# Kernel tuning notes

Hardware: AMD Instinct MI355X
Metric: run time of the kernel (lower is better)

## Reference

```python
import jax, jax.numpy as jnp
import numpy as np

B, G, C = 32, 50, 80
IMG = 640
STRIDES = (8, 16, 32)
CENTER_RADIUS = 2.5


def _make_grids():
    xs, ys, ss = [], [], []
    for s in STRIDES:
        n = IMG // s
        yv, xv = np.meshgrid(np.arange(n, dtype=np.float32), np.arange(n, dtype=np.float32), indexing='ij')
        xs.append(xv.reshape(-1)); ys.append(yv.reshape(-1))
        ss.append(np.full(n * n, s, dtype=np.float32))
    return np.concatenate(xs), np.concatenate(ys), np.concatenate(ss)


def setup_inputs():
    xg, yg, sg = _make_grids()
    A = xg.shape[0]  # 8400
    ks = jax.random.split(jax.random.key(0), 5)
    # decoded box predictions near grid centers (cxcywh, pixel units)
    ctr = jnp.stack([jnp.asarray((xg + 0.5) * sg), jnp.asarray((yg + 0.5) * sg)], -1)[None] \
        + jax.random.normal(ks[0], (B, A, 2)) * 8.0
    wh = jnp.exp(jax.random.normal(ks[1], (B, A, 2)) * 0.5) * jnp.asarray(sg)[None, :, None] * 4.0
    pred_output = jnp.concatenate([ctr, wh, jax.random.normal(ks[2], (B, A, 1 + C))], -1)  # [B,A,85]
    obj_preds = jax.random.normal(ks[3], (B, A, 1))
    cls_preds = jax.random.normal(ks[4], (B, A, C))
    # labels [B,G,5] = (class, cx, cy, w, h); first num_gt rows valid, rest zero
    rng = np.random.RandomState(0)
    lab = np.zeros((B, G, 5), np.float32)
    for b in range(B):
        ng = rng.randint(5, G)
        lab[b, :ng, 0] = rng.randint(0, C, ng)
        lab[b, :ng, 1:3] = rng.uniform(40.0, IMG - 40.0, (ng, 2))
        lab[b, :ng, 3:5] = rng.uniform(20.0, 160.0, (ng, 2))
    return {"pred_output": pred_output, "obj_preds": obj_preds, "cls_preds": cls_preds,
            "labels": jnp.asarray(lab), "x_shifts": jnp.asarray(xg),
            "y_shifts": jnp.asarray(yg), "strides": jnp.asarray(sg)}


def _pairwise_iou_cxcywh(a, b):
    # a [G,4], b [A,4] -> [G,A]
    tl = jnp.maximum(a[:, None, :2] - a[:, None, 2:] * 0.5, b[None, :, :2] - b[None, :, 2:] * 0.5)
    br = jnp.minimum(a[:, None, :2] + a[:, None, 2:] * 0.5, b[None, :, :2] + b[None, :, 2:] * 0.5)
    area_a = a[:, 2] * a[:, 3]
    area_b = b[:, 2] * b[:, 3]
    en = jnp.all(tl < br, -1).astype(a.dtype)
    area_i = jnp.prod(br - tl, -1) * en
    return area_i / (area_a[:, None] + area_b[None, :] - area_i + 1e-16)


def _assign_one(gt, gt_valid, boxes, cls_logit, obj_logit, xg, yg, sg):
    # SimOTA assignment for a single image, fully vectorized over [G,A].
    # gt [G,5], gt_valid [G], boxes [A,4], cls_logit [A,C], obj_logit [A,1]
    num_gt = gt.shape[0]
    gt_cls = gt[:, 0].astype(jnp.int32)
    gb = gt[:, 1:5]
    xc = (xg + 0.5) * sg
    yc = (yg + 0.5) * sg
    d_box = jnp.stack([
        xc[None, :] - (gb[:, 0:1] - gb[:, 2:3] * 0.5),
        (gb[:, 0:1] + gb[:, 2:3] * 0.5) - xc[None, :],
        yc[None, :] - (gb[:, 1:2] - gb[:, 3:4] * 0.5),
        (gb[:, 1:2] + gb[:, 3:4] * 0.5) - yc[None, :]], -1)
    in_boxes = (jnp.min(d_box, -1) > 0) & gt_valid[:, None]
    d_ctr = jnp.stack([
        xc[None, :] - (gb[:, 0:1] - CENTER_RADIUS * sg[None, :]),
        (gb[:, 0:1] + CENTER_RADIUS * sg[None, :]) - xc[None, :],
        yc[None, :] - (gb[:, 1:2] - CENTER_RADIUS * sg[None, :]),
        (gb[:, 1:2] + CENTER_RADIUS * sg[None, :]) - yc[None, :]], -1)
    in_ctr = (jnp.min(d_ctr, -1) > 0) & gt_valid[:, None]
    fg0 = jnp.any(in_boxes | in_ctr, 0)           # [A] candidate anchors (fg_mask)
    and_ctr = in_boxes & in_ctr                    # [G,A]
    ious = _pairwise_iou_cxcywh(gb, boxes) * fg0[None, :].astype(boxes.dtype) * gt_valid[:, None].astype(boxes.dtype)
    # pairwise BCE(sqrt(sig(cls)*sig(obj)), one_hot) summed over classes, without [G,A,C]
    logq = 0.5 * (jax.nn.log_sigmoid(cls_logit) + jax.nn.log_sigmoid(obj_logit))  # [A,C]
    q = jnp.clip(jnp.exp(logq), 1e-7, 1.0 - 1e-7)
    s_neg = jnp.sum(jnp.log1p(-q), -1)             # [A] sum_c log(1-q_c)
    q_gt = q[:, gt_cls].T                          # [G,A]
    cls_cost = -jnp.log(q_gt) + jnp.log1p(-q_gt) - s_neg[None, :]
    invalid = (~fg0)[None, :] | (~gt_valid)[:, None]
    cost = cls_cost - 3.0 * jnp.log(ious + 1e-8) + 1e5 * (~and_ctr) + 1e9 * invalid
    # dynamic-k: sum of top-10 ious per gt, truncated, min 1
    dyn_k = jnp.maximum(jnp.sum(jax.lax.top_k(ious, 10)[0], -1).astype(jnp.int32), 1)  # [G]
    ranks = jnp.argsort(jnp.argsort(cost, 1), 1)   # rank of each anchor in ascending cost
    matching = (ranks < dyn_k[:, None]) & gt_valid[:, None]
    # resolve anchors claimed by >1 gt: keep min-cost gt
    best_gt = jnp.argmin(cost, 0)                  # [A]
    onehot_best = jnp.arange(num_gt)[:, None] == best_gt[None, :]
    matching = jnp.where(jnp.sum(matching, 0)[None, :] > 1, onehot_best, matching)
    fg = jnp.any(matching, 0)                      # [A] final fg mask
    matched = jnp.argmax(matching, 0)              # [A] matched gt index
    pred_iou = jnp.sum(matching * ious, 0)         # [A]
    cls_t = jax.nn.one_hot(gt_cls[matched], cls_logit.shape[-1], dtype=boxes.dtype) \
        * (pred_iou * fg.astype(boxes.dtype))[:, None]
    return cls_t, fg, matched


def _forward(pred_output, obj_preds, cls_preds, labels, x_shifts, y_shifts, strides):
    bbox = pred_output[:, :, :4]
    gt_valid = labels.sum(-1) > 0
    cls_t, fg, matched = jax.vmap(_assign_one, in_axes=(0, 0, 0, 0, 0, None, None, None))(
        labels, gt_valid, bbox, cls_preds, obj_preds, x_shifts, y_shifts, strides)
    cls_t = jax.lax.stop_gradient(cls_t)  # get_assignments is @torch.no_grad()
    reg_t = jnp.take_along_axis(labels[:, :, 1:5], matched[:, :, None], axis=1)  # [B,A,4]
    fg_f = fg.astype(pred_output.dtype)
    num_fg = jnp.maximum(jnp.sum(fg_f), 1.0)
    # IoU loss (cxcywh), loss = 1 - iou^2, only on fg anchors
    tl = jnp.maximum(bbox[..., :2] - bbox[..., 2:] * 0.5, reg_t[..., :2] - reg_t[..., 2:] * 0.5)
    br = jnp.minimum(bbox[..., :2] + bbox[..., 2:] * 0.5, reg_t[..., :2] + reg_t[..., 2:] * 0.5)
    en = jnp.all(tl < br, -1).astype(bbox.dtype)
    area_i = jnp.prod(br - tl, -1) * en
    area_u = bbox[..., 2] * bbox[..., 3] + reg_t[..., 2] * reg_t[..., 3] - area_i
    iou = area_i / (area_u + 1e-16)
    loss_iou = jnp.sum((1.0 - iou ** 2) * fg_f) / num_fg
    bce = lambda x, y: jax.nn.softplus(x) - x * y  # BCEWithLogits, reduction='none'
    loss_obj = jnp.sum(bce(obj_preds[..., 0], fg_f)) / num_fg
    loss_cls = jnp.sum(bce(cls_preds, cls_t) * fg_f[..., None]) / num_fg
    return 5.0 * loss_iou + loss_obj + loss_cls


def reference(pred_output, obj_preds, cls_preds, labels, x_shifts, y_shifts, strides):
    return _forward(pred_output, obj_preds, cls_preds, labels, x_shifts, y_shifts, strides)
```

## Files before the change

kernel.cpp:

```cpp
#include <hip/hip_runtime.h>
#include <cstdint>
#include <cstddef>

#define BB 32
#define GG 50
#define CC 80
#define AA 8400
#define PCH (5 + CC)
#define NLB ((BB * AA + 255) / 256)
#define FGBIT 63
#define SENTC 3.3e38f
#define SENTI 0x7fffffff

__device__ __forceinline__ float logsig_fast(float x) {
    float e = __expf(-fabsf(x));
    return fminf(x, 0.f) - __logf(1.f + e);
}
__device__ __forceinline__ float softplusf(float x) {
    return fmaxf(x, 0.f) + log1pf(expf(-fabsf(x)));
}

__device__ __forceinline__ float pair_iou(float px, float py, float pw, float ph,
                                          float gx, float gy, float gw, float gh) {
    float tlx = fmaxf(gx - gw * 0.5f, px - pw * 0.5f);
    float tly = fmaxf(gy - gh * 0.5f, py - ph * 0.5f);
    float brx = fminf(gx + gw * 0.5f, px + pw * 0.5f);
    float bry = fminf(gy + gh * 0.5f, py + ph * 0.5f);
    float en = (tlx < brx && tly < bry) ? 1.f : 0.f;
    float ai = (brx - tlx) * (bry - tly) * en;
    return ai / (gw * gh + pw * ph - ai + 1e-16f);
}
__device__ __forceinline__ float cost_val(float x , float lo ,
                                          float sn , float v ,
                                          bool ac, bool f0, bool valid) {
    float lq = 0.5f * (logsig_fast(x) + lo);
    float q = fminf(fmaxf(__expf(lq), 1e-7f), 1.f - 1e-7f);
    float cst = -__logf(q) + __logf(1.f - q) - sn;
    cst -= 3.0f * __logf(v + 1e-8f);
    cst += 100000.0f * (ac ? 0.f : 1.f);
    cst += 1000000000.0f * ((!f0 || !valid) ? 1.f : 0.f);
    return cst;
}

__global__ void k_geom(const float* __restrict__ labels, const float* __restrict__ xs,
                       const float* __restrict__ ys, const float* __restrict__ ss,
                       const float* __restrict__ pred,
                       unsigned long long* __restrict__ amask,
                       int* __restrict__ clist, unsigned long long* __restrict__ camask,
                       float4* __restrict__ cpbox, int* __restrict__ ccnt) {
    int b = blockIdx.y;
    int a = blockIdx.x * blockDim.x + threadIdx.x;
    __shared__ float lab[GG * 5];
    __shared__ int lv[GG];
    for (int t = threadIdx.x; t < GG * 5; t += blockDim.x) lab[t] = labels[b * GG * 5 + t];
    __syncthreads();
    if (threadIdx.x < GG) {
        const float* r = lab + threadIdx.x * 5;
        lv[threadIdx.x] = ((r[0] + r[1] + r[2] + r[3] + r[4]) > 0.f) ? 1 : 0;
    }
    __syncthreads();
    if (a >= AA) return;
    float s = ss[a];
    float xc = (xs[a] + 0.5f) * s;
    float yc = (ys[a] + 0.5f) * s;
    unsigned long long m = 0;
    int any = 0;
    for (int g = 0; g < GG; g++) {
        if (!lv[g]) continue;
        const float* r = lab + g * 5;
        float gx = r[1], gy = r[2], gw = r[3], gh = r[4];
        float d1 = xc - (gx - gw * 0.5f);
        float d2 = (gx + gw * 0.5f) - xc;
        float d3 = yc - (gy - gh * 0.5f);
        float d4 = (gy + gh * 0.5f) - yc;
        bool ib = fminf(fminf(d1, d2), fminf(d3, d4)) > 0.f;
        float cr = 2.5f * s;
        float e1 = xc - (gx - cr);
        float e2 = (gx + cr) - xc;
        float e3 = yc - (gy - cr);
        float e4 = (gy + cr) - yc;
        bool ic = fminf(fminf(e1, e2), fminf(e3, e4)) > 0.f;
        if (ib || ic) any = 1;
        if (ib && ic) m |= 1ull << g;
    }
    if (any) m |= 1ull << FGBIT;
    amask[b * AA + a] = m;
    int lane = threadIdx.x & 63;
    unsigned long long act = __ballot(m != 0);
    if (act) {
        int leader = __ffsll(act) - 1;
        int base = 0;
        if (lane == leader) base = atomicAdd(&ccnt[b], __popcll(act));
        base = __shfl(base, leader);
        if (m != 0) {
            int off = __popcll(act & ((1ull << lane) - 1ull));
            int pos = b * AA + base + off;
            clist[pos] = a;
            camask[pos] = m;
            const float* p = pred + (size_t)(b * AA + a) * PCH;
            cpbox[pos] = make_float4(p[0], p[1], p[2], p[3]);
        }
    }
}

__global__ __launch_bounds__(256)
void k_pre_fg(const float* __restrict__ obj, const float* __restrict__ cls,
              const int* __restrict__ clist, const int* __restrict__ ccnt,
              float2* __restrict__ clsn, float2* __restrict__ lsn,
              float* __restrict__ sps) {
    int b = blockIdx.y;
    int cnt = ccnt[b];
    int t = blockIdx.x * blockDim.x + threadIdx.x;
    int p = t >> 2;
    int sub = t & 3;
    if (p >= cnt) return;
    int pos = b * AA + p;
    int a = clist[pos];
    int ia = b * AA + a;
    float lo = logsig_fast(obj[ia]);
    float K = __expf(0.5f * lo);
    const float4* c4 = (const float4*)(cls + (size_t)ia * CC);
    float smax = 0.f, psp = 1.f, p1 = 1.f, p2 = 1.f;
#pragma unroll
    for (int j = 0; j < 5; j++) {
        float4 v = c4[sub + 4 * j];
        float xs4[4] = {v.x, v.y, v.z, v.w};
        float pg = 1.f;
#pragma unroll
        for (int u = 0; u < 4; u++) {
            float x = xs4[u];
            float th = __expf(-0.5f * fabsf(x));
            float t2 = th * th;
            smax += fmaxf(x, 0.f);
            psp *= (1.f + t2);
            float qq = K * (x < 0.f ? th : 1.f) * rsqrtf(1.f + t2);
            qq = fminf(fmaxf(qq, 1e-7f), 1.f - 1e-7f);
            pg *= (1.f - qq);
        }
        if (j < 2) p1 *= pg; else p2 *= pg;
    }
    float sp = smax + __logf(psp);
    float sn = __logf(p1) + __logf(p2);
    sp += __shfl_xor(sp, 1); sn += __shfl_xor(sn, 1);
    sp += __shfl_xor(sp, 2); sn += __shfl_xor(sn, 2);
    if (sub == 0) {
        clsn[pos] = make_float2(lo, sn);
        lsn[ia] = make_float2(lo, sn);
        sps[ia] = sp;
    }
}

__global__ __launch_bounds__(256, 4)
void k_assign(const float* __restrict__ pred, const float2* __restrict__ lsn,
              const float* __restrict__ cls,
              const unsigned long long* __restrict__ amask,
              const float* __restrict__ labels,
              const int* __restrict__ clist, const unsigned long long* __restrict__ camask,
              const float4* __restrict__ cpbox, const float2* __restrict__ clsn,
              const int* __restrict__ ccnt,
              unsigned long long* __restrict__ mmask) {
    int w = blockIdx.x;
    int b = w / GG, g = w % GG;
    const float* r = labels + (size_t)w * 5;
    float gcls = r[0], gx = r[1], gy = r[2], gw = r[3], gh = r[4];
    if (!((gcls + gx + gy + gw + gh) > 0.f)) return;
    int gtc = (int)gcls;
    int tid = threadIdx.x;
    int lane = tid & 63;
    int wv = tid >> 6;
    int cnt = ccnt[b];

    float ivl[10];
    float cvl[10];
    int   cil[10];
#pragma unroll
    for (int t = 0; t < 10; t++) { ivl[t] = 0.f; cvl[t] = SENTC; cil[t] = SENTI; }
    int nlc = 0;

    for (int i0 = wv * 64 + lane; i0 < cnt; i0 += 256) {
        int pos = b * AA + i0;
        unsigned long long am = camask[pos];
        float4 pb = cpbox[pos];
        bool ac = (am >> g) & 1ull;
        nlc += ac ? 1 : 0;
        float v = pair_iou(pb.x, pb.y, pb.z, pb.w, gx, gy, gw, gh);
        if (v > ivl[9]) {
            float mv = v;
#pragma unroll
            for (int t = 0; t < 10; t++)
                if (mv > ivl[t]) { float tmp = ivl[t]; ivl[t] = mv; mv = tmp; }
        }
        if (ac) {
            int a = clist[pos];
            float2 ls = clsn[pos];
            float c = cost_val(cls[((size_t)b * AA + a) * CC + gtc], ls.x, ls.y, v,
                               true, true, true);
            int id = a;
            if (c < cvl[9] || (c == cvl[9] && id < cil[9])) {
#pragma unroll
                for (int t = 0; t < 10; t++) {
                    bool sw = (c < cvl[t]) || (c == cvl[t] && id < cil[t]);
                    if (sw) {
                        float tf = cvl[t]; cvl[t] = c; c = tf;
                        int ti = cil[t]; cil[t] = id; id = ti;
                    }
                }
            }
        }
    }

    __shared__ float IV[4][10];
    __shared__ float CV[4][10];
    __shared__ int CI[4][10];
    __shared__ int NAC[4];
    __shared__ int s_k, s_n0;
    __shared__ int sel[10];

    {
        int s = nlc;
#pragma unroll
        for (int off = 1; off < 64; off <<= 1) s += __shfl_xor(s, off);
        if (lane == 0) NAC[wv] = s;
    }

    for (int rr = 0; rr < 10; rr++) {
        float bv = ivl[0];
        int bl = lane;
#pragma unroll
        for (int off = 1; off < 64; off <<= 1) {
            float ov = __shfl_xor(bv, off);
            int ol = __shfl_xor(bl, off);
            if (ov > bv || (ov == bv && ol < bl)) { bv = ov; bl = ol; }
        }
        if (lane == 0) IV[wv][rr] = bv;
        if (lane == bl) {
#pragma unroll
            for (int t = 0; t < 9; t++) ivl[t] = ivl[t + 1];
            ivl[9] = 0.f;
        }
    }

    for (int rr = 0; rr < 10; rr++) {
        float bc = cvl[0];
        int bi = cil[0];
        int bl = lane;
#pragma unroll
        for (int off = 1; off < 64; off <<= 1) {
            float oc = __shfl_xor(bc, off);
            int oi = __shfl_xor(bi, off);
            int ol = __shfl_xor(bl, off);
            bool tk = (oc < bc) || (oc == bc && (oi < bi || (oi == bi && ol < bl)));
            if (tk) { bc = oc; bi = oi; bl = ol; }
        }
        if (lane == 0) { CV[wv][rr] = bc; CI[wv][rr] = bi; }
        if (lane == bl) {
#pragma unroll
            for (int t = 0; t < 9; t++) { cvl[t] = cvl[t + 1]; cil[t] = cil[t + 1]; }
            cvl[9] = SENTC; cil[9] = SENTI;
        }
    }
    __syncthreads();

    if (tid == 0) {
        int h[4] = {0, 0, 0, 0};
        float ssum = 0.f;
        for (int j = 0; j < 10; j++) {
            float bv = -1.f; int bc = 0;
#pragma unroll
            for (int c2 = 0; c2 < 4; c2++)
                if (h[c2] < 10 && IV[c2][h[c2]] > bv) { bv = IV[c2][h[c2]]; bc = c2; }
            ssum += bv;
            h[bc]++;
        }
        int k = (int)ssum;
        if (k < 1) k = 1;
        s_k = k;
        s_n0 = NAC[0] + NAC[1] + NAC[2] + NAC[3];
    }
    __syncthreads();
    int k = s_k;

    if (s_n0 < k) {
#pragma unroll
        for (int t = 0; t < 10; t++) { cvl[t] = SENTC; cil[t] = SENTI; }
        const int chunk = AA / 4;
        int abase = wv * chunk, aend = abase + chunk;
        for (int a0 = abase; a0 < aend; a0 += 64) {
            int a = a0 + lane;
            bool inr = a < aend;
            int ia = b * AA + (inr ? a : (aend - 1));
            unsigned long long am = amask[ia];
            bool f0 = inr && ((am >> FGBIT) & 1ull);
            bool ac = inr && ((am >> g) & 1ull);
            float v = 0.f;
            if (f0) {
                const float* p = pred + (size_t)ia * PCH;
                v = pair_iou(p[0], p[1], p[2], p[3], gx, gy, gw, gh);
            }
            float c = SENTC; int id = SENTI;
            if (inr) {
                float x = cls[(size_t)ia * CC + gtc];
                float2 ls = lsn[ia];
                c = cost_val(x, ls.x, ls.y, v, ac, f0, true);
                id = a;
            }
            if (c < cvl[9] || (c == cvl[9] && id < cil[9])) {
#pragma unroll
                for (int t = 0; t < 10; t++) {
                    bool sw = (c < cvl[t]) || (c == cvl[t] && id < cil[t]);
                    if (sw) {
                        float tf = cvl[t]; cvl[t] = c; c = tf;
                        int ti = cil[t]; cil[t] = id; id = ti;
                    }
                }
            }
        }
        for (int rr = 0; rr < 10; rr++) {
            float bc = cvl[0];
            int bi = cil[0];
            int bl = lane;
#pragma unroll
            for (int off = 1; off < 64; off <<= 1) {
                float oc = __shfl_xor(bc, off);
                int oi = __shfl_xor(bi, off);
                int ol = __shfl_xor(bl, off);
                bool tk = (oc < bc) || (oc == bc && (oi < bi || (oi == bi && ol < bl)));
                if (tk) { bc = oc; bi = oi; bl = ol; }
            }
            if (lane == 0) { CV[wv][rr] = bc; CI[wv][rr] = bi; }
            if (lane == bl) {
#pragma unroll
                for (int t = 0; t < 9; t++) { cvl[t] = cvl[t + 1]; cil[t] = cil[t + 1]; }
                cvl[9] = SENTC; cil[9] = SENTI;
            }
        }
        __syncthreads();
    }

    if (tid == 0) {
        int h[4] = {0, 0, 0, 0};
        for (int j = 0; j < k; j++) {
            float bv = SENTC; int bix = SENTI; int bc = 0;
#pragma unroll
            for (int c2 = 0; c2 < 4; c2++) {
                if (h[c2] < 10) {
                    float av = CV[c2][h[c2]]; int ax = CI[c2][h[c2]];
                    if (av < bv || (av == bv && ax < bix)) { bv = av; bix = ax; bc = c2; }
                }
            }
            sel[j] = bix;
            h[bc]++;
        }
    }
    __syncthreads();
    if (tid < k) {
        atomicOr(&mmask[(size_t)b * AA + sel[tid]], 1ull << g);
    }
}

__global__ void k_loss(const float* __restrict__ pred, const float* __restrict__ obj,
                       const float* __restrict__ cls, const float* __restrict__ labels,
                       const float2* __restrict__ lsn,
                       const unsigned long long* __restrict__ amask,
                       const unsigned long long* __restrict__ mmask,
                       const float* __restrict__ sps, float* __restrict__ partial) {
    int i = blockIdx.x * blockDim.x + threadIdx.x;
    int i_first = blockIdx.x * blockDim.x;
    int i_last = min(i_first + (int)blockDim.x - 1, BB * AA - 1);
    int b0 = i_first / AA, b1 = i_last / AA;
    __shared__ float lab[2][GG * 5];
    for (int t = threadIdx.x; t < GG * 5; t += blockDim.x) {
        lab[0][t] = labels[(size_t)b0 * GG * 5 + t];
        lab[1][t] = labels[(size_t)b1 * GG * 5 + t];
    }
    __syncthreads();

    float li = 0.f, lo = 0.f, lc = 0.f, nf = 0.f;
    if (i < BB * AA) {
        int b = i / AA, a = i % AA;
        const float* lb = lab[(b == b0) ? 0 : 1];
        unsigned long long m = mmask[i];
        int cnt = __popcll(m);
        bool fg = (m != 0);
        int mg = 0;
        float4 pb = make_float4(0.f, 0.f, 0.f, 0.f);
        if (fg) {
            const float* p = pred + (size_t)i * PCH;
            pb = make_float4(p[0], p[1], p[2], p[3]);
        }
        unsigned long long am = amask[i];
        bool f0 = (am >> FGBIT) & 1ull;
        if (cnt > 1) {
            float2 ls = lsn[i];
            float bv = 3.4e38f;
            for (int g = 0; g < GG; g++) {
                const float* r = lb + g * 5;
                float gcls = r[0], gx = r[1], gy = r[2], gw = r[3], gh = r[4];
                bool valid = (gcls + gx + gy + gw + gh) > 0.f;
                int gtc = (int)gcls;
                float raw = pair_iou(pb.x, pb.y, pb.z, pb.w, gx, gy, gw, gh);
                float v = raw * (f0 ? 1.f : 0.f) * (valid ? 1.f : 0.f);
                float x = cls[(size_t)i * CC + gtc];
                bool ac = (am >> g) & 1ull;
                float cst = cost_val(x, ls.x, ls.y, v, ac, f0, valid);
                if (cst < bv) { bv = cst; mg = g; }
            }
        } else if (cnt == 1) {
            mg = __ffsll((unsigned long long)m) - 1;
        }
        float o = obj[i];
        lo = softplusf(o) - (fg ? o : 0.f);
        if (fg) {
            const float* r = lb + mg * 5;
            float gcls = r[0], gx = r[1], gy = r[2], gw = r[3], gh = r[4];
            bool valid = (gcls + gx + gy + gw + gh) > 0.f;
            int gtc = (int)gcls;
            float piou = pair_iou(pb.x, pb.y, pb.z, pb.w, gx, gy, gw, gh)
                         * (f0 ? 1.f : 0.f) * (valid ? 1.f : 0.f);
            float tlx = fmaxf(pb.x - pb.z * 0.5f, gx - gw * 0.5f);
            float tly = fmaxf(pb.y - pb.w * 0.5f, gy - gh * 0.5f);
            float brx = fminf(pb.x + pb.z * 0.5f, gx + gw * 0.5f);
            float bry = fminf(pb.y + pb.w * 0.5f, gy + gh * 0.5f);
            float en = (tlx < brx && tly < bry) ? 1.f : 0.f;
            float ai = (brx - tlx) * (bry - tly) * en;
            float u = pb.z * pb.w + gw * gh - ai;
            float v2 = ai / (u + 1e-16f);
            li = 1.f - v2 * v2;
            lc = sps[i] - cls[(size_t)i * CC + gtc] * piou;
            nf = 1.f;
        }
    }
    for (int off = 32; off; off >>= 1) {
        li += __shfl_down(li, off);
        lo += __shfl_down(lo, off);
        lc += __shfl_down(lc, off);
        nf += __shfl_down(nf, off);
    }
    __shared__ float red[4][4];
    int wid = threadIdx.x >> 6;
    if ((threadIdx.x & 63) == 0) {
        red[wid][0] = li; red[wid][1] = lo; red[wid][2] = lc; red[wid][3] = nf;
    }
    __syncthreads();
    if (threadIdx.x == 0) {
        float s0 = 0.f, s1 = 0.f, s2 = 0.f, s3 = 0.f;
#pragma unroll
        for (int t = 0; t < 4; t++) {
            s0 += red[t][0]; s1 += red[t][1]; s2 += red[t][2]; s3 += red[t][3];
        }
        ((float4*)partial)[blockIdx.x] = make_float4(s0, s1, s2, s3);
    }
}

__global__ void k_final(const float* __restrict__ partial, float* __restrict__ out) {
    int tid = threadIdx.x;
    float s0 = 0.f, s1 = 0.f, s2 = 0.f, s3 = 0.f;
    const float4* pb = (const float4*)partial;
    for (int i = tid; i < NLB; i += 256) {
        float4 v = pb[i];
        s0 += v.x; s1 += v.y; s2 += v.z; s3 += v.w;
    }
    for (int off = 32; off; off >>= 1) {
        s0 += __shfl_down(s0, off);
        s1 += __shfl_down(s1, off);
        s2 += __shfl_down(s2, off);
        s3 += __shfl_down(s3, off);
    }
    __shared__ float red[4][4];
    int wid = tid >> 6;
    if ((tid & 63) == 0) {
        red[wid][0] = s0; red[wid][1] = s1; red[wid][2] = s2; red[wid][3] = s3;
    }
    __syncthreads();
    if (tid == 0) {
        float li = 0.f, lo = 0.f, lc = 0.f, nf = 0.f;
#pragma unroll
        for (int t = 0; t < 4; t++) {
            li += red[t][0]; lo += red[t][1]; lc += red[t][2]; nf += red[t][3];
        }
        nf = fmaxf(nf, 1.f);
        out[0] = (5.f * li + lo + lc) / nf;
    }
}

extern "C" void kernel_launch(void* const* d_in, const int* in_sizes, int n_in,
                              void* d_out, int out_size, void* d_ws, size_t ws_size,
                              hipStream_t stream) {
    const float* pred = (const float*)d_in[0];
    const float* obj  = (const float*)d_in[1];
    const float* cls  = (const float*)d_in[2];
    const float* lab  = (const float*)d_in[3];
    const float* xs   = (const float*)d_in[4];
    const float* ys   = (const float*)d_in[5];
    const float* ss   = (const float*)d_in[6];
    float* out = (float*)d_out;

    const size_t BA = (size_t)BB * AA;

    float4* cpbox = (float4*)d_ws;
    float2* lsn   = (float2*)(cpbox + BA);
    float2* clsn  = lsn + BA;
    unsigned long long* amask  = (unsigned long long*)(clsn + BA);
    unsigned long long* camask = amask + BA;
    unsigned long long* mmask  = camask + BA;
    float* sps = (float*)(mmask + BA);
    float* partial = sps + BA;
    int* clist = (int*)(partial + (size_t)NLB * 4);
    int* ccnt  = clist + BA;

    hipMemsetAsync(mmask, 0, BA * sizeof(unsigned long long), stream);
    hipMemsetAsync(ccnt, 0, BB * sizeof(int), stream);

    dim3 blk(256);
    k_geom<<<dim3((AA + 255) / 256, BB), blk, 0, stream>>>(lab, xs, ys, ss, pred,
                                                           amask, clist, camask, cpbox,
                                                           ccnt);
    k_pre_fg<<<dim3((AA * 4 + 255) / 256, BB), blk, 0, stream>>>(obj, cls, clist, ccnt,
                                                                 clsn, lsn, sps);
    k_assign<<<dim3(BB * GG), blk, 0, stream>>>(pred, lsn, cls, amask, lab,
                                                clist, camask, cpbox, clsn, ccnt, mmask);
    k_loss<<<dim3(NLB), blk, 0, stream>>>(pred, obj, cls, lab, lsn, amask,
                                          mmask, sps, partial);
    k_final<<<1, blk, 0, stream>>>(partial, out);
}
```

Measured before the change: 143.2 us.

## Split per-GT assignment into two-half scan plus merge kernel

The per-GT dynamic-k assignment kernel is split into two kernels. The first scans the candidate list in two halves with a 2D grid (doubling block count) and writes per-half top-10 IoU and cost lists to workspace. The second, a single-wave block per GT, merges the two halves, computes k, and runs the rare fallback full scan with one wave. The aim is more parallelism in the candidate scan, at the cost of an extra launch, workspace round-trip, and a slower single-wave fallback path.

```diff
diff --git a/kernel.cpp b/kernel.cpp
--- a/kernel.cpp
+++ b/kernel.cpp
@@ -151,15 +151,15 @@
 }
 
 __global__ __launch_bounds__(256, 4)
-void k_assign(const float* __restrict__ pred, const float2* __restrict__ lsn,
-              const float* __restrict__ cls,
-              const unsigned long long* __restrict__ amask,
-              const float* __restrict__ labels,
-              const int* __restrict__ clist, const unsigned long long* __restrict__ camask,
-              const float4* __restrict__ cpbox, const float2* __restrict__ clsn,
-              const int* __restrict__ ccnt,
-              unsigned long long* __restrict__ mmask) {
+void k_assign1(const float* __restrict__ cls,
+               const unsigned long long* __restrict__ camask,
+               const float4* __restrict__ cpbox, const float2* __restrict__ clsn,
+               const int* __restrict__ clist, const int* __restrict__ ccnt,
+               const float* __restrict__ labels,
+               float* __restrict__ giou, float* __restrict__ gcost,
+               int* __restrict__ gidx, int* __restrict__ gnac) {
     int w = blockIdx.x;
+    int half = blockIdx.y;
     int b = w / GG, g = w % GG;
     const float* r = labels + (size_t)w * 5;
     float gcls = r[0], gx = r[1], gy = r[2], gw = r[3], gh = r[4];
@@ -169,6 +169,9 @@
     int lane = tid & 63;
     int wv = tid >> 6;
     int cnt = ccnt[b];
+    int hmid = (cnt + 1) >> 1;
+    int hstart = half ? hmid : 0;
+    int hend = half ? cnt : hmid;
 
     float ivl[10];
     float cvl[10];
@@ -177,7 +180,7 @@
     for (int t = 0; t < 10; t++) { ivl[t] = 0.f; cvl[t] = SENTC; cil[t] = SENTI; }
     int nlc = 0;
 
-    for (int i0 = wv * 64 + lane; i0 < cnt; i0 += 256) {
+    for (int i0 = hstart + wv * 64 + lane; i0 < hend; i0 += 256) {
         int pos = b * AA + i0;
         unsigned long long am = camask[pos];
         float4 pb = cpbox[pos];
@@ -213,8 +216,6 @@
     __shared__ float CV[4][10];
     __shared__ int CI[4][10];
     __shared__ int NAC[4];
-    __shared__ int s_k, s_n0;
-    __shared__ int sel[10];
 
     {
         int s = nlc;
@@ -239,7 +240,6 @@
             ivl[9] = 0.f;
         }
     }
-
     for (int rr = 0; rr < 10; rr++) {
         float bc = cvl[0];
         int bi = cil[0];
@@ -262,48 +262,102 @@
     __syncthreads();
 
     if (tid == 0) {
+        size_t obase = ((size_t)w * 2 + half) * 10;
         int h[4] = {0, 0, 0, 0};
+        for (int j = 0; j < 10; j++) {
+            float bv = -1.f; int bc = 0;
+#pragma unroll
+            for (int c2 = 0; c2 < 4; c2++)
+                if (h[c2] < 10 && IV[c2][h[c2]] > bv) { bv = IV[c2][h[c2]]; bc = c2; }
+            giou[obase + j] = bv;
+            h[bc]++;
+        }
+        h[0] = h[1] = h[2] = h[3] = 0;
+        for (int j = 0; j < 10; j++) {
+            float bv = SENTC; int bix = SENTI; int bc = 0;
+#pragma unroll
+            for (int c2 = 0; c2 < 4; c2++) {
+                if (h[c2] < 10) {
+                    float av = CV[c2][h[c2]]; int ax = CI[c2][h[c2]];
+                    if (av < bv || (av == bv && ax < bix)) { bv = av; bix = ax; bc = c2; }
+                }
+            }
+            gcost[obase + j] = bv;
+            gidx[obase + j] = bix;
+            h[bc]++;
+        }
+        gnac[w * 2 + half] = NAC[0] + NAC[1] + NAC[2] + NAC[3];
+    }
+}
+
+__global__ __launch_bounds__(64)
+void k_assign2(const float* __restrict__ labels,
+               const float* __restrict__ giou, const float* __restrict__ gcost,
+               const int* __restrict__ gidx, const int* __restrict__ gnac,
+               const float* __restrict__ pred, const float2* __restrict__ lsn,
+               const float* __restrict__ cls,
+               const unsigned long long* __restrict__ amask,
+               unsigned long long* __restrict__ mmask) {
+    int w = blockIdx.x;
+    int b = w / GG, g = w % GG;
+    const float* r = labels + (size_t)w * 5;
+    float gcls = r[0], gx = r[1], gy = r[2], gw = r[3], gh = r[4];
+    if (!((gcls + gx + gy + gw + gh) > 0.f)) return;
+    int gtc = (int)gcls;
+    int lane = threadIdx.x;
+
+    __shared__ int s_k, s_n0;
+    __shared__ int sel[10];
+
+    if (lane == 0) {
+        size_t o0 = (size_t)w * 2 * 10, o1 = o0 + 10;
+        int h0 = 0, h1 = 0;
         float ssum = 0.f;
         for (int j = 0; j < 10; j++) {
-            float bv = -1.f; int bc = 0;
-#pragma unroll
-            for (int c2 = 0; c2 < 4; c2++)
-                if (h[c2] < 10 && IV[c2][h[c2]] > bv) { bv = IV[c2][h[c2]]; bc = c2; }
-            ssum += bv;
-            h[bc]++;
+            float a0 = (h0 < 10) ? giou[o0 + h0] : -1.f;
+            float a1 = (h1 < 10) ? giou[o1 + h1] : -1.f;
+            if (a0 >= a1) { ssum += a0; h0++; }
+            else          { ssum += a1; h1++; }
         }
         int k = (int)ssum;
         if (k < 1) k = 1;
         s_k = k;
-        s_n0 = NAC[0] + NAC[1] + NAC[2] + NAC[3];
+        s_n0 = gnac[w * 2] + gnac[w * 2 + 1];
+        if (s_n0 >= k) {
+            h0 = h1 = 0;
+            for (int j = 0; j < k; j++) {
+                float a0 = (h0 < 10) ? gcost[o0 + h0] : SENTC;
+                int x0 = (h0 < 10) ? gidx[o0 + h0] : SENTI;
+                float a1 = (h1 < 10) ? gcost[o1 + h1] : SENTC;
+                int x1 = (h1 < 10) ? gidx[o1 + h1] : SENTI;
+                bool t0 = (a0 < a1) || (a0 == a1 && x0 < x1);
+                if (t0) { sel[j] = x0; h0++; }
+                else    { sel[j] = x1; h1++; }
+            }
+        }
     }
     __syncthreads();
     int k = s_k;
 
     if (s_n0 < k) {
+        float cvl[10];
+        int cil[10];
 #pragma unroll
         for (int t = 0; t < 10; t++) { cvl[t] = SENTC; cil[t] = SENTI; }
-        const int chunk = AA / 4;
-        int abase = wv * chunk, aend = abase + chunk;
-        for (int a0 = abase; a0 < aend; a0 += 64) {
-            int a = a0 + lane;
-            bool inr = a < aend;
-            int ia = b * AA + (inr ? a : (aend - 1));
+        for (int a = lane; a < AA; a += 64) {
+            int ia = b * AA + a;
             unsigned long long am = amask[ia];
-            bool f0 = inr && ((am >> FGBIT) & 1ull);
-            bool ac = inr && ((am >> g) & 1ull);
+            bool f0 = (am >> FGBIT) & 1ull;
+            bool ac = (am >> g) & 1ull;
             float v = 0.f;
             if (f0) {
                 const float* p = pred + (size_t)ia * PCH;
                 v = pair_iou(p[0], p[1], p[2], p[3], gx, gy, gw, gh);
             }
-            float c = SENTC; int id = SENTI;
-            if (inr) {
-                float x = cls[(size_t)ia * CC + gtc];
-                float2 ls = lsn[ia];
-                c = cost_val(x, ls.x, ls.y, v, ac, f0, true);
-                id = a;
-            }
+            float x = cls[(size_t)ia * CC + gtc];
+            float2 ls = lsn[ia];
+            float c = cost_val(x, ls.x, ls.y, v, ac, f0, true);
+            int id = a;
             if (c < cvl[9] || (c == cvl[9] && id < cil[9])) {
 #pragma unroll
                 for (int t = 0; t < 10; t++) {
@@ -315,7 +369,7 @@
                 }
             }
         }
-        for (int rr = 0; rr < 10; rr++) {
+        for (int rr = 0; rr < k; rr++) {
             float bc = cvl[0];
             int bi = cil[0];
             int bl = lane;
@@ -327,7 +381,7 @@
                 bool tk = (oc < bc) || (oc == bc && (oi < bi || (oi == bi && ol < bl)));
                 if (tk) { bc = oc; bi = oi; bl = ol; }
             }
-            if (lane == 0) { CV[wv][rr] = bc; CI[wv][rr] = bi; }
+            if (lane == 0) sel[rr] = bi;
             if (lane == bl) {
 #pragma unroll
                 for (int t = 0; t < 9; t++) { cvl[t] = cvl[t + 1]; cil[t] = cil[t + 1]; }
@@ -337,24 +391,8 @@
         __syncthreads();
     }
 
-    if (tid == 0) {
-        int h[4] = {0, 0, 0, 0};
-        for (int j = 0; j < k; j++) {
-            float bv = SENTC; int bix = SENTI; int bc = 0;
-#pragma unroll
-            for (int c2 = 0; c2 < 4; c2++) {
-                if (h[c2] < 10) {
-                    float av = CV[c2][h[c2]]; int ax = CI[c2][h[c2]];
-                    if (av < bv || (av == bv && ax < bix)) { bv = av; bix = ax; bc = c2; }
-                }
-            }
-            sel[j] = bix;
-            h[bc]++;
-        }
-    }
-    __syncthreads();
-    if (tid < k) {
-        atomicOr(&mmask[(size_t)b * AA + sel[tid]], 1ull << g);
+    if (lane < k) {
+        atomicOr(&mmask[(size_t)b * AA + sel[lane]], 1ull << g);
     }
 }
 
@@ -496,6 +534,7 @@
     float* out = (float*)d_out;
 
     const size_t BA = (size_t)BB * AA;
+    const size_t WH = (size_t)BB * GG * 2;
 
     float4* cpbox = (float4*)d_ws;
     float2* lsn   = (float2*)(cpbox + BA);
@@ -507,6 +546,10 @@
     float* partial = sps + BA;
     int* clist = (int*)(partial + (size_t)NLB * 4);
     int* ccnt  = clist + BA;
+    float* giou = (float*)(ccnt + BB);
+    float* gcost = giou + WH * 10;
+    int* gidx = (int*)(gcost + WH * 10);
+    int* gnac = gidx + WH * 10;
 
     hipMemsetAsync(mmask, 0, BA * sizeof(unsigned long long), stream);
     hipMemsetAsync(ccnt, 0, BB * sizeof(int), stream);
@@ -517,8 +560,10 @@
                                                            ccnt);
     k_pre_fg<<<dim3((AA * 4 + 255) / 256, BB), blk, 0, stream>>>(obj, cls, clist, ccnt,
                                                                  clsn, lsn, sps);
-    k_assign<<<dim3(BB * GG), blk, 0, stream>>>(pred, lsn, cls, amask, lab,
-                                                clist, camask, cpbox, clsn, ccnt, mmask);
+    k_assign1<<<dim3(BB * GG, 2), blk, 0, stream>>>(cls, camask, cpbox, clsn, clist,
+                                                    ccnt, lab, giou, gcost, gidx, gnac);
+    k_assign2<<<dim3(BB * GG), dim3(64), 0, stream>>>(lab, giou, gcost, gidx, gnac,
+                                                      pred, lsn, cls, amask, mmask);
     k_loss<<<dim3(NLB), blk, 0, stream>>>(pred, obj, cls, lab, lsn, amask,
                                           mmask, sps, partial);
     k_final<<<1, blk, 0, stream>>>(partial, out);
```

Measured after the change: 155.1 us. 1.08x slower.
